# Kernel optimization log

Measured on AMD Instinct MI355X. Metric: run time of the kernel, lower is better.

Reference implementation:

```python
import jax, jax.numpy as jnp
import numpy as np

B, WIN, NN, F_IN, H = 8, 12, 2000, 8, 64
N = B * WIN * NN          # total graph nodes = 192000
E = 2_000_000             # edges
EPS = 1e-5                # BatchNorm eps
FC1_IN = 2 * H + WIN * F_IN + 1  # 225


def setup_inputs() -> dict:
    key = jax.random.key(0)
    ks = jax.random.split(key, 24)
    s = lambda k, shp: (jax.random.normal(k, shp, jnp.float32) * 0.05)
    d = {}
    d["adj_indices"] = jax.random.randint(ks[0], (2, E), 0, N)
    d["adj_weight"] = jax.random.uniform(ks[1], (E,), jnp.float32)
    d["x"] = jax.random.normal(ks[2], (N, F_IN), jnp.float32)
    d["inner_out"] = jax.random.normal(ks[3], (B * NN,), jnp.float32)
    # GCN layers
    d["W1"] = s(ks[4], (F_IN, H)); d["b1"] = jnp.zeros((H,), jnp.float32)
    d["W2"] = s(ks[5], (H, H));    d["b2"] = jnp.zeros((H,), jnp.float32)
    # BatchNorm affine params
    d["g1"] = jnp.ones((H,), jnp.float32);  d["be1"] = jnp.zeros((H,), jnp.float32)
    d["g2"] = jnp.ones((H,), jnp.float32);  d["be2"] = jnp.zeros((H,), jnp.float32)
    # LSTM 1 (input 2H) and LSTM 2 (input H); torch gate order i,f,g,o
    d["Wih1"] = s(ks[6], (4 * H, 2 * H)); d["Whh1"] = s(ks[7], (4 * H, H))
    d["bih1"] = jnp.zeros((4 * H,), jnp.float32); d["bhh1"] = jnp.zeros((4 * H,), jnp.float32)
    d["Wih2"] = s(ks[8], (4 * H, H)); d["Whh2"] = s(ks[9], (4 * H, H))
    d["bih2"] = jnp.zeros((4 * H,), jnp.float32); d["bhh2"] = jnp.zeros((4 * H,), jnp.float32)
    # FC head
    d["fc1_w"] = s(ks[10], (FC1_IN, H)); d["fc1_b"] = jnp.zeros((H,), jnp.float32)
    d["fc3_w"] = s(ks[11], (H, 1));      d["fc3_b"] = jnp.zeros((1,), jnp.float32)
    return d


def gcn(x, W, b, row, col, w):
    # PyG GCNConv: add self loops (weight 1), symmetric deg^-1/2 normalization,
    # aggregate messages from row (source) into col (target).
    loop = jnp.arange(N)
    r = jnp.concatenate([row, loop])
    c = jnp.concatenate([col, loop])
    ww = jnp.concatenate([w, jnp.ones((N,), w.dtype)])
    deg = jax.ops.segment_sum(ww, c, num_segments=N)
    dis = jnp.where(deg > 0, 1.0 / jnp.sqrt(deg), 0.0)
    norm = dis[r] * ww * dis[c]                      # [E+N]
    h = x @ W                                        # [N,H]
    out = jax.ops.segment_sum(h[r] * norm[:, None], c, num_segments=N)
    return out + b


def bn(x, g, b):  # training-mode BatchNorm1d (batch stats, biased var)
    m = x.mean(0)
    v = x.var(0)
    return (x - m) / jnp.sqrt(v + EPS) * g + b


def lstm(xs, Wih, Whh, bih, bhh):
    # xs: [T, Bn, D]; returns (all hidden states [T,Bn,H], last hidden [Bn,H])
    Bn = xs.shape[1]
    h0 = jnp.zeros((Bn, H), xs.dtype)
    def step(carry, xt):
        h, c = carry
        gates = xt @ Wih.T + h @ Whh.T + bih + bhh
        i, f, g, o = jnp.split(gates, 4, axis=-1)
        c = jax.nn.sigmoid(f) * c + jax.nn.sigmoid(i) * jnp.tanh(g)
        h = jax.nn.sigmoid(o) * jnp.tanh(c)
        return (h, c), h
    (hT, _), ys = jax.lax.scan(step, (h0, h0), xs)
    return ys, hT


def reference(adj_indices, adj_weight, x, inner_out,
              W1, b1, W2, b2, g1, be1, g2, be2,
              Wih1, Whh1, bih1, bhh1, Wih2, Whh2, bih2, bhh2,
              fc1_w, fc1_b, fc3_w, fc3_b):
    row, col = adj_indices[0], adj_indices[1]
    skip = x.reshape(B, WIN, NN, F_IN).transpose(0, 2, 1, 3).reshape(B * NN, WIN * F_IN)
    h1 = bn(jax.nn.relu(gcn(x, W1, b1, row, col, adj_weight)), g1, be1)   # dropout = identity (eval)
    h2 = bn(jax.nn.relu(gcn(h1, W2, b2, row, col, adj_weight)), g2, be2)
    h = jnp.concatenate([h1, h2], axis=1)                                  # [N, 2H]
    seq = h.reshape(B, WIN, NN, 2 * H).transpose(1, 0, 2, 3).reshape(WIN, B * NN, 2 * H)
    y1, hn1 = lstm(seq, Wih1, Whh1, bih1, bhh1)
    _, hn2 = lstm(y1, Wih2, Whh2, bih2, bhh2)
    z = jnp.concatenate([hn1, hn2, inner_out[:, None], skip], axis=1)      # [B*NN, FC1_IN]
    z = jax.nn.relu(z @ fc1_w + fc1_b)
    z = jax.nn.relu(z @ fc3_w + fc3_b)
    return z.reshape(-1)                                                   # [B*NN]
```

## Files before the change

kernel.cpp:

```cpp
#include <hip/hip_runtime.h>
#include <math.h>

#define N_NODES 192000
#define EDGES   2000000
#define HID     64
#define BN_ROWS 16000
#define T_WIN   12
#define B_SZ    8
#define NN_SZ   2000
#define FIN     8
#define BN_EPS  1e-5f

#define NBKT    750
#define NBLKA   1024
#define ACHUNK  1956
#define BKT_CAP 5120

typedef _Float16 f16x2 __attribute__((ext_vector_type(2)));
typedef _Float16 half4 __attribute__((ext_vector_type(4)));
typedef _Float16 half8 __attribute__((ext_vector_type(8)));
typedef float    f32x4 __attribute__((ext_vector_type(4)));
union F16x2U { float f; f16x2 h; };

__device__ __forceinline__ float frcp(float x){
#if __has_builtin(__builtin_amdgcn_rcpf)
    return __builtin_amdgcn_rcpf(x);
#else
    return 1.0f/x;
#endif
}
__device__ __forceinline__ float fsig(float x){ return frcp(1.0f + __expf(-x)); }
__device__ __forceinline__ float ftanh(float x){ return fmaf(2.0f, fsig(2.0f*x), -1.0f); }

__device__ __forceinline__ float packf16(float a, float b){
    F16x2U u; u.h[0] = (_Float16)a; u.h[1] = (_Float16)b; return u.f;
}

__global__ __launch_bounds__(256) void hist_coarse(
        const int* __restrict__ col, unsigned* __restrict__ gcount,
        int* __restrict__ blockbase){
    __shared__ unsigned bh[NBKT];
    int bl = blockIdx.x, tid = threadIdx.x;
    for (int i = tid; i < NBKT; i += 256) bh[i] = 0u;
    __syncthreads();
    int e0 = bl*ACHUNK;
    int e1 = e0 + ACHUNK; if (e1 > EDGES) e1 = EDGES;
    for (int e = e0 + tid*4; e < e1; e += 1024){
        int4 c4 = *(const int4*)&col[e];
        atomicAdd(&bh[((unsigned)c4.x) >> 8], 1u);
        atomicAdd(&bh[((unsigned)c4.y) >> 8], 1u);
        atomicAdd(&bh[((unsigned)c4.z) >> 8], 1u);
        atomicAdd(&bh[((unsigned)c4.w) >> 8], 1u);
    }
    __syncthreads();
    for (int i = tid; i < NBKT; i += 256)
        blockbase[bl*NBKT + i] = (int)atomicAdd(&gcount[i], bh[i]);
}

__global__ __launch_bounds__(1024) void scan_bkt(
        const unsigned* __restrict__ gcount, int* __restrict__ gbase,
        int* __restrict__ offsets){
    __shared__ int sm[1024];
    int tid = threadIdx.x;
    int v = (tid < NBKT) ? (int)gcount[tid] : 0;
    sm[tid] = v;
    __syncthreads();
    #pragma unroll
    for (int off = 1; off < 1024; off <<= 1){
        int t = (tid >= off) ? sm[tid - off] : 0;
        __syncthreads();
        sm[tid] += t;
        __syncthreads();
    }
    if (tid < NBKT) gbase[tid] = sm[tid] - v;
    if (tid == NBKT) gbase[NBKT] = EDGES;
    if (tid == NBKT+1) offsets[N_NODES] = EDGES;
}

__global__ __launch_bounds__(256) void scatter_bucket(
        const int* __restrict__ row, const int* __restrict__ col,
        const float* __restrict__ w, const int* __restrict__ blockbase,
        const int* __restrict__ gbase, int2* __restrict__ rec){
    __shared__ unsigned cur[NBKT];
    int bl = blockIdx.x, tid = threadIdx.x;
    for (int i = tid; i < NBKT; i += 256)
        cur[i] = (unsigned)(gbase[i] + blockbase[bl*NBKT + i]);
    __syncthreads();
    int e0 = bl*ACHUNK;
    int e1 = e0 + ACHUNK; if (e1 > EDGES) e1 = EDGES;
    for (int e = e0 + tid*4; e < e1; e += 1024){
        int4 r4 = *(const int4*)&row[e];
        int4 c4 = *(const int4*)&col[e];
        float4 w4 = *(const float4*)&w[e];
        int cc[4] = {c4.x, c4.y, c4.z, c4.w};
        int rr[4] = {r4.x, r4.y, r4.z, r4.w};
        float wf[4] = {w4.x, w4.y, w4.z, w4.w};
        #pragma unroll
        for (int q = 0; q < 4; q++){
            int c = cc[q];
            unsigned wfix = (unsigned)(wf[q]*16777216.0f + 0.5f);
            if (wfix > 0xFFFFFFu) wfix = 0xFFFFFFu;
            unsigned p = atomicAdd(&cur[((unsigned)c) >> 8], 1u);
            int2 rv; rv.x = rr[q];
            rv.y = (int)((((unsigned)(c & 255)) << 24) | wfix);
            rec[p] = rv;
        }
    }
}

__global__ __launch_bounds__(256) void bucket_csr(
        const int2* __restrict__ rec, const int* __restrict__ gbase,
        int2* __restrict__ edge_s, int* __restrict__ offsets,
        float* __restrict__ dis){
    __shared__ int2 S[BKT_CAP];
    __shared__ unsigned cnt[256];
    __shared__ unsigned wsum[256];
    __shared__ unsigned cur[256];
    __shared__ float dloc[256];
    int b = blockIdx.x, tid = threadIdx.x;
    int k0 = gbase[b], k1 = gbase[b+1];
    int n = k1 - k0;
    cnt[tid] = 0u; wsum[tid] = 0u;
    __syncthreads();
    bool staged = (n <= BKT_CAP);
    for (int i = tid; i < n; i += 256){
        int2 r = rec[k0 + i];
        if (staged) S[i] = r;
        unsigned clow = ((unsigned)r.y) >> 24;
        atomicAdd(&cnt[clow], 1u);
        atomicAdd(&wsum[clow], ((unsigned)r.y) & 0xFFFFFFu);
    }
    __syncthreads();
    unsigned v = cnt[tid];
    float deg = (float)wsum[tid] * (1.0f/16777216.0f);
    float dv = rsqrtf(deg + 1.0f);
    dloc[tid] = dv;
    dis[(b<<8) + tid] = dv;
    #pragma unroll
    for (int off = 1; off < 256; off <<= 1){
        unsigned t = (tid >= off) ? cnt[tid - off] : 0u;
        __syncthreads();
        cnt[tid] += t;
        __syncthreads();
    }
    unsigned excl = cnt[tid] - v;
    cur[tid] = excl;
    offsets[(b<<8) + tid] = k0 + (int)excl;
    __syncthreads();
    for (int i = tid; i < n; i += 256){
        int2 r = staged ? S[i] : rec[k0 + i];
        unsigned clow = ((unsigned)r.y) >> 24;
        unsigned wfix = ((unsigned)r.y) & 0xFFFFFFu;
        float sv = (float)wfix * (1.0f/16777216.0f) * dloc[clow];
        unsigned p = atomicAdd(&cur[clow], 1u);
        int2 o; o.x = (int)((clow << 24) | (unsigned)r.x); o.y = __float_as_int(sv);
        edge_s[k0 + (int)p] = o;
    }
}

__global__ __launch_bounds__(256) void edge_fix(
        int2* __restrict__ edge_s, const float* __restrict__ dis){
    int i = blockIdx.x*256 + threadIdx.x;
    if (i >= EDGES) return;
    int2 e = edge_s[i];
    e.y = __float_as_int(dis[e.x & 0xFFFFFF]*__int_as_float(e.y));
    edge_s[i] = e;
}

__global__ __launch_bounds__(256) void aggx_k(
        const int* __restrict__ offsets, const int2* __restrict__ edge_s,
        const float* __restrict__ dis, const float* __restrict__ x,
        float* __restrict__ ax){
    int g   = blockIdx.x*32 + (threadIdx.x >> 3);
    int sub = threadIdx.x & 7;
    float d = dis[g];
    float acc = x[(size_t)g*8 + sub]*d*d;
    int k  = offsets[g];
    int k1 = offsets[g+1];
    for (; k+4 <= k1; k += 4){
        int2 e0 = edge_s[k], e1 = edge_s[k+1], e2 = edge_s[k+2], e3 = edge_s[k+3];
        float v0 = x[(size_t)(e0.x & 0xFFFFFF)*8 + sub];
        float v1 = x[(size_t)(e1.x & 0xFFFFFF)*8 + sub];
        float v2 = x[(size_t)(e2.x & 0xFFFFFF)*8 + sub];
        float v3 = x[(size_t)(e3.x & 0xFFFFFF)*8 + sub];
        acc += v0*__int_as_float(e0.y);
        acc += v1*__int_as_float(e1.y);
        acc += v2*__int_as_float(e2.y);
        acc += v3*__int_as_float(e3.y);
    }
    for (; k < k1; k++){
        int2 e0 = edge_s[k];
        acc += x[(size_t)(e0.x & 0xFFFFFF)*8 + sub]*__int_as_float(e0.y);
    }
    ax[(size_t)g*8 + sub] = acc;
}

__global__ __launch_bounds__(256) void lin1b_stats(
        const float* __restrict__ ax, const float* __restrict__ W1,
        const float* __restrict__ b1, float* __restrict__ out,
        float* __restrict__ gsum, float* __restrict__ gsq){
    __shared__ float Ws[512];
    for (int i = threadIdx.x; i < 512; i += 256) Ws[i] = W1[i];
    __syncthreads();
    int f = threadIdx.x & 63;
    float wc[8];
    #pragma unroll
    for (int q = 0; q < 8; q++) wc[q] = Ws[q*64 + f];
    float bb = b1[f];
    float s = 0.f, s2 = 0.f;
    int stride = gridDim.x*blockDim.x;
    for (int idx = blockIdx.x*blockDim.x + threadIdx.x; idx < N_NODES*64; idx += stride){
        int j = idx >> 6;
        const float* ar = ax + (size_t)j*8;
        float acc = bb;
        #pragma unroll
        for (int q = 0; q < 8; q++) acc += ar[q]*wc[q];
        float v = fmaxf(acc, 0.f);
        out[idx] = v;
        s += v; s2 += v*v;
    }
    __shared__ float s1m[256], s2m[256];
    s1m[threadIdx.x] = s; s2m[threadIdx.x] = s2;
    __syncthreads();
    if (threadIdx.x < 64){
        float t1 = s1m[threadIdx.x]+s1m[threadIdx.x+64]+s1m[threadIdx.x+128]+s1m[threadIdx.x+192];
        float t2 = s2m[threadIdx.x]+s2m[threadIdx.x+64]+s2m[threadIdx.x+128]+s2m[threadIdx.x+192];
        atomicAdd(&gsum[threadIdx.x], t1);
        atomicAdd(&gsq[threadIdx.x], t2);
    }
}

#define L2ROWS 128
#define XS2    132
__global__ __launch_bounds__(128) void lin2_bn(
        const float* __restrict__ gcnA, const float* __restrict__ gsum,
        const float* __restrict__ gsq, const float* __restrict__ g1,
        const float* __restrict__ be1, const float* __restrict__ W2,
        _Float16* __restrict__ h1H, float* __restrict__ hlinH){
    __shared__ float Ws[64*64];
    __shared__ float xsT[64*XS2];
    int tid = threadIdx.x;
    int r0 = blockIdx.x * L2ROWS;

    for (int i = tid; i < 1024; i += 128)
        *(float4*)&Ws[i*4] = *(const float4*)&W2[i*4];

    int k4 = tid & 15;
    int rb = tid >> 4;
    float scv[4], shv[4];
    #pragma unroll
    for (int q = 0; q < 4; q++){
        int f = k4*4 + q;
        float mean = gsum[f]*(1.0f/(float)N_NODES);
        float var  = fmaxf(gsq[f]*(1.0f/(float)N_NODES) - mean*mean, 0.f);
        float sc_  = g1[f]*rsqrtf(var + BN_EPS);
        scv[q] = sc_; shv[q] = be1[f] - mean*sc_;
    }
    for (int it = 0; it < 16; it++){
        int r = it*8 + rb;
        float4 v = *(const float4*)&gcnA[(size_t)(r0+r)*64 + k4*4];
        v.x = v.x*scv[0]+shv[0]; v.y = v.y*scv[1]+shv[1];
        v.z = v.z*scv[2]+shv[2]; v.w = v.w*scv[3]+shv[3];
        half4 hh;
        hh[0]=(_Float16)v.x; hh[1]=(_Float16)v.y; hh[2]=(_Float16)v.z; hh[3]=(_Float16)v.w;
        *(half4*)&h1H[(size_t)(r0+r)*64 + k4*4] = hh;
        xsT[(k4*4+0)*XS2 + r] = v.x;
        xsT[(k4*4+1)*XS2 + r] = v.y;
        xsT[(k4*4+2)*XS2 + r] = v.z;
        xsT[(k4*4+3)*XS2 + r] = v.w;
    }
    __syncthreads();

    int cg = tid & 7;
    int rg = tid >> 3;
    float acc[8][8];
    #pragma unroll
    for (int i = 0; i < 8; i++)
        #pragma unroll
        for (int j = 0; j < 8; j++) acc[i][j] = 0.f;

    float4 a0 = *(float4*)&xsT[0*XS2 + rg*8];
    float4 a1 = *(float4*)&xsT[0*XS2 + rg*8 + 4];
    float4 w0 = *(float4*)&Ws[0*64 + cg*8];
    float4 w1 = *(float4*)&Ws[0*64 + cg*8 + 4];
    for (int k = 0; k < 64; k++){
        float4 na0, na1, nw0, nw1;
        if (k < 63){
            na0 = *(float4*)&xsT[(k+1)*XS2 + rg*8];
            na1 = *(float4*)&xsT[(k+1)*XS2 + rg*8 + 4];
            nw0 = *(float4*)&Ws[(k+1)*64 + cg*8];
            nw1 = *(float4*)&Ws[(k+1)*64 + cg*8 + 4];
        }
        float ar[8] = {a0.x,a0.y,a0.z,a0.w,a1.x,a1.y,a1.z,a1.w};
        float wcv[8] = {w0.x,w0.y,w0.z,w0.w,w1.x,w1.y,w1.z,w1.w};
        #pragma unroll
        for (int i = 0; i < 8; i++)
            #pragma unroll
            for (int j = 0; j < 8; j++) acc[i][j] += ar[i]*wcv[j];
        a0=na0; a1=na1; w0=nw0; w1=nw1;
    }
    #pragma unroll
    for (int i = 0; i < 8; i++){
        size_t r = (size_t)(r0 + rg*8 + i);
        float4 pk;
        pk.x = packf16(acc[i][0], acc[i][1]);
        pk.y = packf16(acc[i][2], acc[i][3]);
        pk.z = packf16(acc[i][4], acc[i][5]);
        pk.w = packf16(acc[i][6], acc[i][7]);
        *(float4*)&hlinH[r*32 + cg*4] = pk;
    }
}

__global__ __launch_bounds__(256) void gather2h(
        const int* __restrict__ offsets, const int2* __restrict__ edge_s,
        const float* __restrict__ dis, const float* __restrict__ hlinH,
        const float* __restrict__ bias, float* __restrict__ g2Hf){
    int j = blockIdx.x*8 + (threadIdx.x >> 5);
    int p = threadIdx.x & 31;
    float d = dis[j];
    float dd = d*d;
    F16x2U u; u.f = hlinH[(size_t)j*32 + p];
    float ax = (float)u.h[0]*dd;
    float ay = (float)u.h[1]*dd;
    int k  = offsets[j];
    int k1 = offsets[j+1];
    for (; k+4 <= k1; k += 4){
        int2 e0 = edge_s[k], e1 = edge_s[k+1], e2 = edge_s[k+2], e3 = edge_s[k+3];
        F16x2U a, b, c, e;
        a.f = hlinH[(size_t)(e0.x & 0xFFFFFF)*32 + p];
        b.f = hlinH[(size_t)(e1.x & 0xFFFFFF)*32 + p];
        c.f = hlinH[(size_t)(e2.x & 0xFFFFFF)*32 + p];
        e.f = hlinH[(size_t)(e3.x & 0xFFFFFF)*32 + p];
        float n0 = __int_as_float(e0.y), n1 = __int_as_float(e1.y);
        float n2 = __int_as_float(e2.y), n3 = __int_as_float(e3.y);
        ax += (float)a.h[0]*n0; ay += (float)a.h[1]*n0;
        ax += (float)b.h[0]*n1; ay += (float)b.h[1]*n1;
        ax += (float)c.h[0]*n2; ay += (float)c.h[1]*n2;
        ax += (float)e.h[0]*n3; ay += (float)e.h[1]*n3;
    }
    for (; k < k1; k++){
        int2 e0 = edge_s[k];
        F16x2U a; a.f = hlinH[(size_t)(e0.x & 0xFFFFFF)*32 + p];
        float n0 = __int_as_float(e0.y);
        ax += (float)a.h[0]*n0; ay += (float)a.h[1]*n0;
    }
    float2 bv = *(const float2*)&bias[2*p];
    float vx = fmaxf(ax + bv.x, 0.f);
    float vy = fmaxf(ay + bv.y, 0.f);
    F16x2U o; o.h[0] = (_Float16)vx; o.h[1] = (_Float16)vy;
    g2Hf[(size_t)j*32 + p] = o.f;
}

__global__ __launch_bounds__(256) void stats2h(
        const float* __restrict__ g2Hf, float* __restrict__ gsum2, float* __restrict__ gsq2){
    int p = threadIdx.x & 31;
    float s0 = 0.f, s1 = 0.f, q0 = 0.f, q1 = 0.f;
    int stride = gridDim.x*blockDim.x;
    for (int idx = blockIdx.x*blockDim.x + threadIdx.x; idx < N_NODES*32; idx += stride){
        F16x2U u; u.f = g2Hf[idx];
        float vx = (float)u.h[0], vy = (float)u.h[1];
        s0 += vx; q0 += vx*vx;
        s1 += vy; q1 += vy*vy;
    }
    __shared__ float sb[128];
    if (threadIdx.x < 128) sb[threadIdx.x] = 0.f;
    __syncthreads();
    atomicAdd(&sb[2*p],      s0);
    atomicAdd(&sb[2*p+1],    s1);
    atomicAdd(&sb[64+2*p],   q0);
    atomicAdd(&sb[64+2*p+1], q1);
    __syncthreads();
    if (threadIdx.x < 64){
        atomicAdd(&gsum2[threadIdx.x], sb[threadIdx.x]);
        atomicAdd(&gsq2[threadIdx.x],  sb[64+threadIdx.x]);
    }
}

__global__ void prep_weights(const float* __restrict__ Wih1, const float* __restrict__ Whh1,
                             const float* __restrict__ bih1, const float* __restrict__ bhh1,
                             const float* __restrict__ Wih2, const float* __restrict__ Whh2,
                             const float* __restrict__ bih2, const float* __restrict__ bhh2,
                             _Float16* W1F, _Float16* W2F, float* b1c, float* b2c){
    int idx = blockIdx.x*blockDim.x + threadIdx.x;
    if (idx < 6*256*32){
        int kt = idx >> 13;
        int rem = idx & 8191;
        int n = rem >> 5, kin = rem & 31;
        int k = kt*32 + kin;
        float v = (k < 128) ? Wih1[n*128 + k] : Whh1[n*64 + (k-128)];
        W1F[idx] = (_Float16)v;
    }
    int i2 = idx - 6*256*32;
    if (i2 >= 0 && i2 < 4*256*32){
        int kt = i2 >> 13;
        int rem = i2 & 8191;
        int n = rem >> 5, kin = rem & 31;
        int k = kt*32 + kin;
        float v = (k < 64) ? Wih2[n*64 + k] : Whh2[n*64 + (k-64)];
        W2F[i2] = (_Float16)v;
    }
    int i3 = idx - (6*256*32 + 4*256*32);
    if (i3 >= 0 && i3 < 256) b1c[i3] = bih1[i3] + bhh1[i3];
    int i4 = i3 - 256;
    if (i4 >= 0 && i4 < 256) b2c[i4] = bih2[i4] + bhh2[i4];
}

#define X1S 200
#define X2S 136
__global__ __launch_bounds__(256) void lstm_fused(
        const _Float16* __restrict__ h1H, const _Float16* __restrict__ g2H,
        const float* __restrict__ gsum2, const float* __restrict__ gsq2,
        const float* __restrict__ g2bn, const float* __restrict__ be2,
        const _Float16* __restrict__ W1F, const _Float16* __restrict__ W2F,
        const float* __restrict__ b1c, const float* __restrict__ b2c,
        float* __restrict__ h1s, float* __restrict__ h2s){
    __shared__ _Float16 X1h[16*X1S];
    __shared__ _Float16 X2h[16*X2S];
    int tid = threadIdx.x;
    int j0 = blockIdx.x*16;
    int w    = tid >> 6;
    int lane = tid & 63;
    int quad = lane >> 4;
    int l16  = lane & 15;
    int u    = 16*w + l16;

    int c4 = tid & 15;
    int sr = (tid >> 4) & 15;
    int sj = j0 + sr;
    int sb = sj / NN_SZ, sn = sj - sb*NN_SZ;
    size_t rbase = ((size_t)(sb*T_WIN)*NN_SZ + sn)*64 + c4*4;
    float sc2v[4], sh2v[4];
    #pragma unroll
    for (int q = 0; q < 4; q++){
        int f = c4*4 + q;
        float mean = gsum2[f]*(1.0f/(float)N_NODES);
        float var  = fmaxf(gsq2[f]*(1.0f/(float)N_NODES) - mean*mean, 0.f);
        float sc_  = g2bn[f]*rsqrtf(var + BN_EPS);
        sc2v[q] = sc_; sh2v[q] = be2[f] - mean*sc_;
    }

    float c1r[4], c2r[4], h2r[4];
    #pragma unroll
    for (int i = 0; i < 4; i++){ c1r[i] = 0.f; c2r[i] = 0.f; h2r[i] = 0.f; }

    float bi1 = b1c[u], bf1 = b1c[64+u], bg1 = b1c[128+u], bo1 = b1c[192+u];
    float bi2 = b2c[u], bf2 = b2c[64+u], bg2 = b2c[128+u], bo2 = b2c[192+u];

    {
        half4 v0 = *(const half4*)&h1H[rbase];
        half4 g4 = *(const half4*)&g2H[rbase];
        half4 v1;
        #pragma unroll
        for (int q = 0; q < 4; q++) v1[q] = (_Float16)((float)g4[q]*sc2v[q] + sh2v[q]);
        *(half4*)&X1h[sr*X1S + c4*4]       = v0;
        *(half4*)&X1h[sr*X1S + 64 + c4*4]  = v1;
        *(half4*)&X1h[sr*X1S + 128 + c4*4] = (half4){0,0,0,0};
    }
    __syncthreads();

    for (int t = 0; t < T_WIN; t++){
        half4 nv0, ng4;
        if (t < T_WIN-1){
            size_t rb = rbase + (size_t)(t+1)*NN_SZ*64;
            nv0 = *(const half4*)&h1H[rb];
            ng4 = *(const half4*)&g2H[rb];
        }

        f32x4 acc[4];
        #pragma unroll
        for (int g = 0; g < 4; g++) acc[g] = (f32x4){0.f,0.f,0.f,0.f};
        #pragma unroll
        for (int kt = 0; kt < 6; kt++){
            half8 a = *(const half8*)&X1h[l16*X1S + kt*32 + quad*8];
            #pragma unroll
            for (int g = 0; g < 4; g++){
                half8 b = *(const half8*)&W1F[(size_t)(kt*256 + 64*g + u)*32 + quad*8];
                acc[g] = __builtin_amdgcn_mfma_f32_16x16x32_f16(a, b, acc[g], 0, 0, 0);
            }
        }
        __syncthreads();

        #pragma unroll
        for (int r = 0; r < 4; r++){
            int rowl = quad*4 + r;
            float gi = acc[0][r] + bi1;
            float gf = acc[1][r] + bf1;
            float gg = acc[2][r] + bg1;
            float go = acc[3][r] + bo1;
            float cn = fsig(gf)*c1r[r] + fsig(gi)*ftanh(gg);
            float hn = fsig(go)*ftanh(cn);
            c1r[r] = cn;
            X2h[rowl*X2S + u]      = (_Float16)hn;
            X2h[rowl*X2S + 64 + u] = (_Float16)h2r[r];
            X1h[rowl*X1S + 128 + u] = (_Float16)hn;
            if (t == T_WIN-1) h1s[(size_t)(j0 + rowl)*64 + u] = hn;
        }
        if (t < T_WIN-1){
            half4 v1;
            #pragma unroll
            for (int q = 0; q < 4; q++) v1[q] = (_Float16)((float)ng4[q]*sc2v[q] + sh2v[q]);
            *(half4*)&X1h[sr*X1S + c4*4]      = nv0;
            *(half4*)&X1h[sr*X1S + 64 + c4*4] = v1;
        }
        __syncthreads();

        f32x4 acc2[4];
        #pragma unroll
        for (int g = 0; g < 4; g++) acc2[g] = (f32x4){0.f,0.f,0.f,0.f};
        #pragma unroll
        for (int kt = 0; kt < 4; kt++){
            half8 a = *(const half8*)&X2h[l16*X2S + kt*32 + quad*8];
            #pragma unroll
            for (int g = 0; g < 4; g++){
                half8 b = *(const half8*)&W2F[(size_t)(kt*256 + 64*g + u)*32 + quad*8];
                acc2[g] = __builtin_amdgcn_mfma_f32_16x16x32_f16(a, b, acc2[g], 0, 0, 0);
            }
        }

        #pragma unroll
        for (int r = 0; r < 4; r++){
            int rowl = quad*4 + r;
            float gi = acc2[0][r] + bi2;
            float gf = acc2[1][r] + bf2;
            float gg = acc2[2][r] + bg2;
            float go = acc2[3][r] + bo2;
            float cn = fsig(gf)*c2r[r] + fsig(gi)*ftanh(gg);
            float hn = fsig(go)*ftanh(cn);
            c2r[r] = cn;
            h2r[r] = hn;
            if (t == T_WIN-1) h2s[(size_t)(j0 + rowl)*64 + u] = hn;
        }
    }
}

__global__ __launch_bounds__(256) void fc_head(
        const float* __restrict__ h1s, const float* __restrict__ h2s,
        const float* __restrict__ inner, const float* __restrict__ x,
        const float* __restrict__ fc1_w, const float* __restrict__ fc1_b,
        const float* __restrict__ fc3_w, const float* __restrict__ fc3_b,
        float* __restrict__ out){
    __shared__ float zsm[4][226];
    int wv = threadIdx.x >> 6;
    int f  = threadIdx.x & 63;
    int j  = blockIdx.x*4 + wv;
    int b = j / NN_SZ, n = j - b*NN_SZ;
    for (int k = f; k < 225; k += 64){
        float v;
        if (k < 64)        v = h1s[j*64 + k];
        else if (k < 128)  v = h2s[j*64 + (k-64)];
        else if (k == 128) v = inner[j];
        else {
            int kk = k - 129;
            int w_ = kk >> 3, ff = kk & 7;
            v = x[((b*T_WIN + w_)*NN_SZ + n)*FIN + ff];
        }
        zsm[wv][k] = v;
    }
    __syncthreads();
    float acc = fc1_b[f];
    for (int k = 0; k < 225; k++) acc += zsm[wv][k]*fc1_w[k*64 + f];
    float p = fmaxf(acc, 0.f) * fc3_w[f];
    #pragma unroll
    for (int off = 32; off > 0; off >>= 1) p += __shfl_down(p, off, 64);
    if (f == 0) out[j] = fmaxf(p + fc3_b[0], 0.f);
}

extern "C" void kernel_launch(void* const* d_in, const int* in_sizes, int n_in,
                              void* d_out, int out_size, void* d_ws, size_t ws_size,
                              hipStream_t stream){
    const int*   adj  = (const int*)d_in[0];
    const int*   row  = adj;
    const int*   col  = adj + EDGES;
    const float* aw   = (const float*)d_in[1];
    const float* x    = (const float*)d_in[2];
    const float* inner= (const float*)d_in[3];
    const float* W1   = (const float*)d_in[4];
    const float* b1   = (const float*)d_in[5];
    const float* W2   = (const float*)d_in[6];
    const float* b2   = (const float*)d_in[7];
    const float* g1   = (const float*)d_in[8];
    const float* be1  = (const float*)d_in[9];
    const float* g2   = (const float*)d_in[10];
    const float* be2  = (const float*)d_in[11];
    const float* Wih1 = (const float*)d_in[12];
    const float* Whh1 = (const float*)d_in[13];
    const float* bih1 = (const float*)d_in[14];
    const float* bhh1 = (const float*)d_in[15];
    const float* Wih2 = (const float*)d_in[16];
    const float* Whh2 = (const float*)d_in[17];
    const float* bih2 = (const float*)d_in[18];
    const float* bhh2 = (const float*)d_in[19];
    const float* fc1w = (const float*)d_in[20];
    const float* fc1b = (const float*)d_in[21];
    const float* fc3w = (const float*)d_in[22];
    const float* fc3b = (const float*)d_in[23];
    float* out = (float*)d_out;

    float* ws = (float*)d_ws;
    const size_t NB = (size_t)N_NODES*64;
    float* bufX = ws;
    float* bufY = ws + NB;
    float* bufZ = ws + 2*NB;
    int2*  edge_s  = (int2*)(ws + 3*NB);
    float* degdis  = ws + 3*NB + (size_t)2*EDGES;
    float* gsum    = degdis + N_NODES;
    float* gsq     = gsum + 64;
    float* gsum2   = gsq + 64;
    float* gsq2    = gsum2 + 64;
    unsigned* gcount = (unsigned*)(gsq2 + 64);
    int* gbase   = (int*)(gcount + NBKT);
    int* offsets = gbase + (NBKT + 2);

    int* blockbase = (int*)bufX;
    int2* rec      = (int2*)bufY;

    float* hlinH = bufX;
    _Float16* h1H = (_Float16*)bufZ;
    float* ax    = bufZ + (size_t)N_NODES*32 + 64;
    float* gcnA1 = bufY;
    float* g2Hf  = bufY;

    float* h1s = bufX;
    float* h2s = bufX + (size_t)BN_ROWS*64;
    _Float16* W1F = (_Float16*)(bufX + (size_t)4*BN_ROWS*64);
    _Float16* W2F = W1F + 6*256*32;
    float* b1c = (float*)(W2F + 4*256*32);
    float* b2c = b1c + 256;

    hipMemsetAsync(gcount, 0, NBKT*sizeof(unsigned), stream);
    hipMemsetAsync(gsum, 0, 256*sizeof(float), stream);
    hist_coarse   <<<NBLKA, 256, 0, stream>>>(col, gcount, blockbase);
    scan_bkt      <<<1, 1024, 0, stream>>>(gcount, gbase, offsets);
    scatter_bucket<<<NBLKA, 256, 0, stream>>>(row, col, aw, blockbase, gbase, rec);
    bucket_csr    <<<NBKT, 256, 0, stream>>>(rec, gbase, edge_s, offsets, degdis);
    edge_fix      <<<(EDGES+255)/256, 256, 0, stream>>>(edge_s, degdis);

    aggx_k<<<N_NODES/32, 256, 0, stream>>>(offsets, edge_s, degdis, x, ax);
    lin1b_stats<<<1024, 256, 0, stream>>>(ax, W1, b1, gcnA1, gsum, gsq);

    lin2_bn<<<N_NODES/L2ROWS, 128, 0, stream>>>(gcnA1, gsum, gsq, g1, be1, W2, h1H, hlinH);

    gather2h<<<N_NODES/8, 256, 0, stream>>>(offsets, edge_s, degdis, hlinH, b2, g2Hf);
    stats2h<<<1024, 256, 0, stream>>>(g2Hf, gsum2, gsq2);

    prep_weights<<<(6*256*32 + 4*256*32 + 512 + 255)/256, 256, 0, stream>>>(
        Wih1, Whh1, bih1, bhh1, Wih2, Whh2, bih2, bhh2, W1F, W2F, b1c, b2c);
    lstm_fused<<<BN_ROWS/16, 256, 0, stream>>>(h1H, (const _Float16*)g2Hf,
                                               gsum2, gsq2, g2, be2,
                                               W1F, W2F, b1c, b2c, h1s, h2s);

    fc_head<<<BN_ROWS/4, 256, 0, stream>>>(h1s, h2s, inner, x, fc1w, fc1b, fc3w, fc3b, out);
}
```

Measured before the change: 519.4 us.

## Split degree pass, fold edge_fix into CSR build, double LSTM rows per block

Degree computation moves into its own bucket_deg kernel. bucket_csr can then apply both source and target normalisation when it writes each edge, which removes the separate edge_fix pass over all edges. The LSTM kernel now handles 32 nodes per block instead of 16, so each weight fragment loaded for the MFMAs is reused across two row tiles. The scatter/histogram grid also shrinks from 1024 to 256 blocks with larger chunks, which gives fewer blocks on the GPU and more register and LDS pressure per LSTM block.

```diff
diff --git a/kernel.cpp b/kernel.cpp
--- a/kernel.cpp
+++ b/kernel.cpp
@@ -12,8 +12,8 @@
 #define BN_EPS  1e-5f
 
 #define NBKT    750
-#define NBLKA   1024
-#define ACHUNK  1956
+#define NBLKA   256
+#define ACHUNK  7824
 #define BKT_CAP 5120
 
 typedef _Float16 f16x2 __attribute__((ext_vector_type(2)));
@@ -108,34 +108,45 @@
     }
 }
 
+__global__ __launch_bounds__(256) void bucket_deg(
+        const int2* __restrict__ rec, const int* __restrict__ gbase,
+        float* __restrict__ dis){
+    __shared__ unsigned wsum[256];
+    int b = blockIdx.x, tid = threadIdx.x;
+    wsum[tid] = 0u;
+    __syncthreads();
+    int k0 = gbase[b], k1 = gbase[b+1];
+    for (int i = k0 + tid; i < k1; i += 256){
+        int2 r = rec[i];
+        atomicAdd(&wsum[((unsigned)r.y) >> 24], ((unsigned)r.y) & 0xFFFFFFu);
+    }
+    __syncthreads();
+    float deg = (float)wsum[tid] * (1.0f/16777216.0f);
+    dis[(b<<8) + tid] = rsqrtf(deg + 1.0f);
+}
+
 __global__ __launch_bounds__(256) void bucket_csr(
         const int2* __restrict__ rec, const int* __restrict__ gbase,
-        int2* __restrict__ edge_s, int* __restrict__ offsets,
-        float* __restrict__ dis){
+        const float* __restrict__ dis,
+        int2* __restrict__ edge_s, int* __restrict__ offsets){
     __shared__ int2 S[BKT_CAP];
     __shared__ unsigned cnt[256];
-    __shared__ unsigned wsum[256];
     __shared__ unsigned cur[256];
     __shared__ float dloc[256];
     int b = blockIdx.x, tid = threadIdx.x;
     int k0 = gbase[b], k1 = gbase[b+1];
     int n = k1 - k0;
-    cnt[tid] = 0u; wsum[tid] = 0u;
+    cnt[tid] = 0u;
+    dloc[tid] = dis[(b<<8) + tid];
     __syncthreads();
     bool staged = (n <= BKT_CAP);
     for (int i = tid; i < n; i += 256){
         int2 r = rec[k0 + i];
         if (staged) S[i] = r;
-        unsigned clow = ((unsigned)r.y) >> 24;
-        atomicAdd(&cnt[clow], 1u);
-        atomicAdd(&wsum[clow], ((unsigned)r.y) & 0xFFFFFFu);
+        atomicAdd(&cnt[((unsigned)r.y) >> 24], 1u);
     }
     __syncthreads();
     unsigned v = cnt[tid];
-    float deg = (float)wsum[tid] * (1.0f/16777216.0f);
-    float dv = rsqrtf(deg + 1.0f);
-    dloc[tid] = dv;
-    dis[(b<<8) + tid] = dv;
     #pragma unroll
     for (int off = 1; off < 256; off <<= 1){
         unsigned t = (tid >= off) ? cnt[tid - off] : 0u;
@@ -152,19 +163,11 @@
         unsigned clow = ((unsigned)r.y) >> 24;
         unsigned wfix = ((unsigned)r.y) & 0xFFFFFFu;
         float sv = (float)wfix * (1.0f/16777216.0f) * dloc[clow];
+        sv = dis[r.x] * sv;
         unsigned p = atomicAdd(&cur[clow], 1u);
         int2 o; o.x = (int)((clow << 24) | (unsigned)r.x); o.y = __float_as_int(sv);
         edge_s[k0 + (int)p] = o;
     }
-}
-
-__global__ __launch_bounds__(256) void edge_fix(
-        int2* __restrict__ edge_s, const float* __restrict__ dis){
-    int i = blockIdx.x*256 + threadIdx.x;
-    if (i >= EDGES) return;
-    int2 e = edge_s[i];
-    e.y = __float_as_int(dis[e.x & 0xFFFFFF]*__int_as_float(e.y));
-    edge_s[i] = e;
 }
 
 __global__ __launch_bounds__(256) void aggx_k(
@@ -414,10 +417,10 @@
         const _Float16* __restrict__ W1F, const _Float16* __restrict__ W2F,
         const float* __restrict__ b1c, const float* __restrict__ b2c,
         float* __restrict__ h1s, float* __restrict__ h2s){
-    __shared__ _Float16 X1h[16*X1S];
-    __shared__ _Float16 X2h[16*X2S];
+    __shared__ _Float16 X1h[32*X1S];
+    __shared__ _Float16 X2h[32*X2S];
     int tid = threadIdx.x;
-    int j0 = blockIdx.x*16;
+    int j0 = blockIdx.x*32;
     int w    = tid >> 6;
     int lane = tid & 63;
     int quad = lane >> 4;
@@ -426,9 +429,13 @@
 
     int c4 = tid & 15;
     int sr = (tid >> 4) & 15;
-    int sj = j0 + sr;
-    int sb = sj / NN_SZ, sn = sj - sb*NN_SZ;
-    size_t rbase = ((size_t)(sb*T_WIN)*NN_SZ + sn)*64 + c4*4;
+    int sjA = j0 + sr;
+    int sjB = sjA + 16;
+    int sbA = sjA / NN_SZ, snA = sjA - sbA*NN_SZ;
+    int sbB = sjB / NN_SZ, snB = sjB - sbB*NN_SZ;
+    size_t rbaseA = ((size_t)(sbA*T_WIN)*NN_SZ + snA)*64 + c4*4;
+    size_t rbaseB = ((size_t)(sbB*T_WIN)*NN_SZ + snB)*64 + c4*4;
+    const size_t tstep = (size_t)NN_SZ*64;
     float sc2v[4], sh2v[4];
     #pragma unroll
     for (int q = 0; q < 4; q++){
@@ -439,96 +446,128 @@
         sc2v[q] = sc_; sh2v[q] = be2[f] - mean*sc_;
     }
 
-    float c1r[4], c2r[4], h2r[4];
-    #pragma unroll
-    for (int i = 0; i < 4; i++){ c1r[i] = 0.f; c2r[i] = 0.f; h2r[i] = 0.f; }
+    float c1r[2][4], c2r[2][4], h2r[2][4];
+    #pragma unroll
+    for (int tle = 0; tle < 2; tle++)
+        #pragma unroll
+        for (int i = 0; i < 4; i++){ c1r[tle][i] = 0.f; c2r[tle][i] = 0.f; h2r[tle][i] = 0.f; }
 
     float bi1 = b1c[u], bf1 = b1c[64+u], bg1 = b1c[128+u], bo1 = b1c[192+u];
     float bi2 = b2c[u], bf2 = b2c[64+u], bg2 = b2c[128+u], bo2 = b2c[192+u];
 
     {
-        half4 v0 = *(const half4*)&h1H[rbase];
-        half4 g4 = *(const half4*)&g2H[rbase];
-        half4 v1;
-        #pragma unroll
-        for (int q = 0; q < 4; q++) v1[q] = (_Float16)((float)g4[q]*sc2v[q] + sh2v[q]);
-        *(half4*)&X1h[sr*X1S + c4*4]       = v0;
-        *(half4*)&X1h[sr*X1S + 64 + c4*4]  = v1;
-        *(half4*)&X1h[sr*X1S + 128 + c4*4] = (half4){0,0,0,0};
+        half4 v0A = *(const half4*)&h1H[rbaseA];
+        half4 g4A = *(const half4*)&g2H[rbaseA];
+        half4 v0B = *(const half4*)&h1H[rbaseB];
+        half4 g4B = *(const half4*)&g2H[rbaseB];
+        half4 v1A, v1B;
+        #pragma unroll
+        for (int q = 0; q < 4; q++){
+            v1A[q] = (_Float16)((float)g4A[q]*sc2v[q] + sh2v[q]);
+            v1B[q] = (_Float16)((float)g4B[q]*sc2v[q] + sh2v[q]);
+        }
+        *(half4*)&X1h[sr*X1S + c4*4]             = v0A;
+        *(half4*)&X1h[sr*X1S + 64 + c4*4]        = v1A;
+        *(half4*)&X1h[sr*X1S + 128 + c4*4]       = (half4){0,0,0,0};
+        *(half4*)&X1h[(sr+16)*X1S + c4*4]        = v0B;
+        *(half4*)&X1h[(sr+16)*X1S + 64 + c4*4]   = v1B;
+        *(half4*)&X1h[(sr+16)*X1S + 128 + c4*4]  = (half4){0,0,0,0};
     }
     __syncthreads();
 
     for (int t = 0; t < T_WIN; t++){
-        half4 nv0, ng4;
+        half4 nv0A, ng4A, nv0B, ng4B;
         if (t < T_WIN-1){
-            size_t rb = rbase + (size_t)(t+1)*NN_SZ*64;
-            nv0 = *(const half4*)&h1H[rb];
-            ng4 = *(const half4*)&g2H[rb];
-        }
-
-        f32x4 acc[4];
-        #pragma unroll
-        for (int g = 0; g < 4; g++) acc[g] = (f32x4){0.f,0.f,0.f,0.f};
+            size_t rbA = rbaseA + (size_t)(t+1)*tstep;
+            size_t rbB = rbaseB + (size_t)(t+1)*tstep;
+            nv0A = *(const half4*)&h1H[rbA];
+            ng4A = *(const half4*)&g2H[rbA];
+            nv0B = *(const half4*)&h1H[rbB];
+            ng4B = *(const half4*)&g2H[rbB];
+        }
+
+        f32x4 acc[2][4];
+        #pragma unroll
+        for (int tle = 0; tle < 2; tle++)
+            #pragma unroll
+            for (int g = 0; g < 4; g++) acc[tle][g] = (f32x4){0.f,0.f,0.f,0.f};
         #pragma unroll
         for (int kt = 0; kt < 6; kt++){
-            half8 a = *(const half8*)&X1h[l16*X1S + kt*32 + quad*8];
+            half8 a0 = *(const half8*)&X1h[l16*X1S + kt*32 + quad*8];
+            half8 a1 = *(const half8*)&X1h[(l16+16)*X1S + kt*32 + quad*8];
             #pragma unroll
             for (int g = 0; g < 4; g++){
                 half8 b = *(const half8*)&W1F[(size_t)(kt*256 + 64*g + u)*32 + quad*8];
-                acc[g] = __builtin_amdgcn_mfma_f32_16x16x32_f16(a, b, acc[g], 0, 0, 0);
+                acc[0][g] = __builtin_amdgcn_mfma_f32_16x16x32_f16(a0, b, acc[0][g], 0, 0, 0);
+                acc[1][g] = __builtin_amdgcn_mfma_f32_16x16x32_f16(a1, b, acc[1][g], 0, 0, 0);
             }
         }
         __syncthreads();
 
         #pragma unroll
-        for (int r = 0; r < 4; r++){
-            int rowl = quad*4 + r;
-            float gi = acc[0][r] + bi1;
-            float gf = acc[1][r] + bf1;
-            float gg = acc[2][r] + bg1;
-            float go = acc[3][r] + bo1;
-            float cn = fsig(gf)*c1r[r] + fsig(gi)*ftanh(gg);
-            float hn = fsig(go)*ftanh(cn);
-            c1r[r] = cn;
-            X2h[rowl*X2S + u]      = (_Float16)hn;
-            X2h[rowl*X2S + 64 + u] = (_Float16)h2r[r];
-            X1h[rowl*X1S + 128 + u] = (_Float16)hn;
-            if (t == T_WIN-1) h1s[(size_t)(j0 + rowl)*64 + u] = hn;
+        for (int tle = 0; tle < 2; tle++){
+            #pragma unroll
+            for (int r = 0; r < 4; r++){
+                int rowl = quad*4 + r + 16*tle;
+                float gi = acc[tle][0][r] + bi1;
+                float gf = acc[tle][1][r] + bf1;
+                float gg = acc[tle][2][r] + bg1;
+                float go = acc[tle][3][r] + bo1;
+                float cn = fsig(gf)*c1r[tle][r] + fsig(gi)*ftanh(gg);
+                float hn = fsig(go)*ftanh(cn);
+                c1r[tle][r] = cn;
+                X2h[rowl*X2S + u]      = (_Float16)hn;
+                X2h[rowl*X2S + 64 + u] = (_Float16)h2r[tle][r];
+                X1h[rowl*X1S + 128 + u] = (_Float16)hn;
+                if (t == T_WIN-1) h1s[(size_t)(j0 + rowl)*64 + u] = hn;
+            }
         }
         if (t < T_WIN-1){
-            half4 v1;
-            #pragma unroll
-            for (int q = 0; q < 4; q++) v1[q] = (_Float16)((float)ng4[q]*sc2v[q] + sh2v[q]);
-            *(half4*)&X1h[sr*X1S + c4*4]      = nv0;
-            *(half4*)&X1h[sr*X1S + 64 + c4*4] = v1;
+            half4 v1A, v1B;
+            #pragma unroll
+            for (int q = 0; q < 4; q++){
+                v1A[q] = (_Float16)((float)ng4A[q]*sc2v[q] + sh2v[q]);
+                v1B[q] = (_Float16)((float)ng4B[q]*sc2v[q] + sh2v[q]);
+            }
+            *(half4*)&X1h[sr*X1S + c4*4]            = nv0A;
+            *(half4*)&X1h[sr*X1S + 64 + c4*4]       = v1A;
+            *(half4*)&X1h[(sr+16)*X1S + c4*4]       = nv0B;
+            *(half4*)&X1h[(sr+16)*X1S + 64 + c4*4]  = v1B;
         }
         __syncthreads();
 
-        f32x4 acc2[4];
-        #pragma unroll
-        for (int g = 0; g < 4; g++) acc2[g] = (f32x4){0.f,0.f,0.f,0.f};
+        f32x4 acc2[2][4];
+        #pragma unroll
+        for (int tle = 0; tle < 2; tle++)
+            #pragma unroll
+            for (int g = 0; g < 4; g++) acc2[tle][g] = (f32x4){0.f,0.f,0.f,0.f};
         #pragma unroll
         for (int kt = 0; kt < 4; kt++){
-            half8 a = *(const half8*)&X2h[l16*X2S + kt*32 + quad*8];
+            half8 a0 = *(const half8*)&X2h[l16*X2S + kt*32 + quad*8];
+            half8 a1 = *(const half8*)&X2h[(l16+16)*X2S + kt*32 + quad*8];
             #pragma unroll
             for (int g = 0; g < 4; g++){
                 half8 b = *(const half8*)&W2F[(size_t)(kt*256 + 64*g + u)*32 + quad*8];
-                acc2[g] = __builtin_amdgcn_mfma_f32_16x16x32_f16(a, b, acc2[g], 0, 0, 0);
+                acc2[0][g] = __builtin_amdgcn_mfma_f32_16x16x32_f16(a0, b, acc2[0][g], 0, 0, 0);
+                acc2[1][g] = __builtin_amdgcn_mfma_f32_16x16x32_f16(a1, b, acc2[1][g], 0, 0, 0);
             }
         }
 
         #pragma unroll
-        for (int r = 0; r < 4; r++){
-            int rowl = quad*4 + r;
-            float gi = acc2[0][r] + bi2;
-            float gf = acc2[1][r] + bf2;
-            float gg = acc2[2][r] + bg2;
-            float go = acc2[3][r] + bo2;
-            float cn = fsig(gf)*c2r[r] + fsig(gi)*ftanh(gg);
-            float hn = fsig(go)*ftanh(cn);
-            c2r[r] = cn;
-            h2r[r] = hn;
-            if (t == T_WIN-1) h2s[(size_t)(j0 + rowl)*64 + u] = hn;
+        for (int tle = 0; tle < 2; tle++){
+            #pragma unroll
+            for (int r = 0; r < 4; r++){
+                int rowl = quad*4 + r + 16*tle;
+                float gi = acc2[tle][0][r] + bi2;
+                float gf = acc2[tle][1][r] + bf2;
+                float gg = acc2[tle][2][r] + bg2;
+                float go = acc2[tle][3][r] + bo2;
+                float cn = fsig(gf)*c2r[tle][r] + fsig(gi)*ftanh(gg);
+                float hn = fsig(go)*ftanh(cn);
+                c2r[tle][r] = cn;
+                h2r[tle][r] = hn;
+                if (t == T_WIN-1) h2s[(size_t)(j0 + rowl)*64 + u] = hn;
+            }
         }
     }
 }
@@ -632,8 +671,8 @@
     hist_coarse   <<<NBLKA, 256, 0, stream>>>(col, gcount, blockbase);
     scan_bkt      <<<1, 1024, 0, stream>>>(gcount, gbase, offsets);
     scatter_bucket<<<NBLKA, 256, 0, stream>>>(row, col, aw, blockbase, gbase, rec);
-    bucket_csr    <<<NBKT, 256, 0, stream>>>(rec, gbase, edge_s, offsets, degdis);
-    edge_fix      <<<(EDGES+255)/256, 256, 0, stream>>>(edge_s, degdis);
+    bucket_deg    <<<NBKT, 256, 0, stream>>>(rec, gbase, degdis);
+    bucket_csr    <<<NBKT, 256, 0, stream>>>(rec, gbase, degdis, edge_s, offsets);
 
     aggx_k<<<N_NODES/32, 256, 0, stream>>>(offsets, edge_s, degdis, x, ax);
     lin1b_stats<<<1024, 256, 0, stream>>>(ax, W1, b1, gcnA1, gsum, gsq);
@@ -645,7 +684,7 @@
 
     prep_weights<<<(6*256*32 + 4*256*32 + 512 + 255)/256, 256, 0, stream>>>(
         Wih1, Whh1, bih1, bhh1, Wih2, Whh2, bih2, bhh2, W1F, W2F, b1c, b2c);
-    lstm_fused<<<BN_ROWS/16, 256, 0, stream>>>(h1H, (const _Float16*)g2Hf,
+    lstm_fused<<<BN_ROWS/32, 256, 0, stream>>>(h1H, (const _Float16*)g2Hf,
                                                gsum2, gsq2, g2, be2,
                                                W1F, W2F, b1c, b2c, h1s, h2s);
 
```

Result: faster. 489.4 us (-5.8%).

## Split degree pass, fold edge_fix into CSR build, register-resident LSTM weights

Applied to the files above, without the earlier changes.

Computes node degrees in a separate bucket_deg pass so bucket_csr can apply both source and target normalization directly, which removes the edge_fix kernel's extra read-write pass over the edge array. It also launches fewer, larger blocks for the histogram and scatter kernels. The LSTM kernel now handles 32 rows per 512-thread block, with each wave keeping half of the gate weights in registers and swapping partial gate results through shared memory. This cuts repeated global weight loads but adds a barrier per step, more register pressure and more LDS use.

```diff
diff --git a/kernel.cpp b/kernel.cpp
--- a/kernel.cpp
+++ b/kernel.cpp
@@ -12,8 +12,8 @@
 #define BN_EPS  1e-5f
 
 #define NBKT    750
-#define NBLKA   1024
-#define ACHUNK  1956
+#define NBLKA   256
+#define ACHUNK  7824
 #define BKT_CAP 5120
 
 typedef _Float16 f16x2 __attribute__((ext_vector_type(2)));
@@ -108,34 +108,45 @@
     }
 }
 
+__global__ __launch_bounds__(256) void bucket_deg(
+        const int2* __restrict__ rec, const int* __restrict__ gbase,
+        float* __restrict__ dis){
+    __shared__ unsigned wsum[256];
+    int b = blockIdx.x, tid = threadIdx.x;
+    wsum[tid] = 0u;
+    __syncthreads();
+    int k0 = gbase[b], k1 = gbase[b+1];
+    for (int i = k0 + tid; i < k1; i += 256){
+        int2 r = rec[i];
+        atomicAdd(&wsum[((unsigned)r.y) >> 24], ((unsigned)r.y) & 0xFFFFFFu);
+    }
+    __syncthreads();
+    float deg = (float)wsum[tid] * (1.0f/16777216.0f);
+    dis[(b<<8) + tid] = rsqrtf(deg + 1.0f);
+}
+
 __global__ __launch_bounds__(256) void bucket_csr(
         const int2* __restrict__ rec, const int* __restrict__ gbase,
-        int2* __restrict__ edge_s, int* __restrict__ offsets,
-        float* __restrict__ dis){
+        const float* __restrict__ dis,
+        int2* __restrict__ edge_s, int* __restrict__ offsets){
     __shared__ int2 S[BKT_CAP];
     __shared__ unsigned cnt[256];
-    __shared__ unsigned wsum[256];
     __shared__ unsigned cur[256];
     __shared__ float dloc[256];
     int b = blockIdx.x, tid = threadIdx.x;
     int k0 = gbase[b], k1 = gbase[b+1];
     int n = k1 - k0;
-    cnt[tid] = 0u; wsum[tid] = 0u;
+    cnt[tid] = 0u;
+    dloc[tid] = dis[(b<<8) + tid];
     __syncthreads();
     bool staged = (n <= BKT_CAP);
     for (int i = tid; i < n; i += 256){
         int2 r = rec[k0 + i];
         if (staged) S[i] = r;
-        unsigned clow = ((unsigned)r.y) >> 24;
-        atomicAdd(&cnt[clow], 1u);
-        atomicAdd(&wsum[clow], ((unsigned)r.y) & 0xFFFFFFu);
+        atomicAdd(&cnt[((unsigned)r.y) >> 24], 1u);
     }
     __syncthreads();
     unsigned v = cnt[tid];
-    float deg = (float)wsum[tid] * (1.0f/16777216.0f);
-    float dv = rsqrtf(deg + 1.0f);
-    dloc[tid] = dv;
-    dis[(b<<8) + tid] = dv;
     #pragma unroll
     for (int off = 1; off < 256; off <<= 1){
         unsigned t = (tid >= off) ? cnt[tid - off] : 0u;
@@ -152,19 +163,11 @@
         unsigned clow = ((unsigned)r.y) >> 24;
         unsigned wfix = ((unsigned)r.y) & 0xFFFFFFu;
         float sv = (float)wfix * (1.0f/16777216.0f) * dloc[clow];
+        sv = dis[r.x] * sv;
         unsigned p = atomicAdd(&cur[clow], 1u);
         int2 o; o.x = (int)((clow << 24) | (unsigned)r.x); o.y = __float_as_int(sv);
         edge_s[k0 + (int)p] = o;
     }
-}
-
-__global__ __launch_bounds__(256) void edge_fix(
-        int2* __restrict__ edge_s, const float* __restrict__ dis){
-    int i = blockIdx.x*256 + threadIdx.x;
-    if (i >= EDGES) return;
-    int2 e = edge_s[i];
-    e.y = __float_as_int(dis[e.x & 0xFFFFFF]*__int_as_float(e.y));
-    edge_s[i] = e;
 }
 
 __global__ __launch_bounds__(256) void aggx_k(
@@ -407,28 +410,35 @@
 
 #define X1S 200
 #define X2S 136
-__global__ __launch_bounds__(256) void lstm_fused(
+#define EXS 130
+__global__ __launch_bounds__(512) void lstm_fused(
         const _Float16* __restrict__ h1H, const _Float16* __restrict__ g2H,
         const float* __restrict__ gsum2, const float* __restrict__ gsq2,
         const float* __restrict__ g2bn, const float* __restrict__ be2,
         const _Float16* __restrict__ W1F, const _Float16* __restrict__ W2F,
         const float* __restrict__ b1c, const float* __restrict__ b2c,
         float* __restrict__ h1s, float* __restrict__ h2s){
-    __shared__ _Float16 X1h[16*X1S];
-    __shared__ _Float16 X2h[16*X2S];
+    __shared__ _Float16 X1h[32*X1S];
+    __shared__ _Float16 X2h[32*X2S];
+    __shared__ float EX1[32*EXS];
+    __shared__ float EX2[32*EXS];
     int tid = threadIdx.x;
-    int j0 = blockIdx.x*16;
+    int j0 = blockIdx.x*32;
     int w    = tid >> 6;
     int lane = tid & 63;
     int quad = lane >> 4;
     int l16  = lane & 15;
-    int u    = 16*w + l16;
-
+    int ug   = w & 3;
+    int gp   = w >> 2;
+    int u    = ug*16 + l16;
+    int row0 = gp*16 + quad*4;
+
+    int sr = tid >> 4;
     int c4 = tid & 15;
-    int sr = (tid >> 4) & 15;
     int sj = j0 + sr;
     int sb = sj / NN_SZ, sn = sj - sb*NN_SZ;
     size_t rbase = ((size_t)(sb*T_WIN)*NN_SZ + sn)*64 + c4*4;
+    const size_t tstep = (size_t)NN_SZ*64;
     float sc2v[4], sh2v[4];
     #pragma unroll
     for (int q = 0; q < 4; q++){
@@ -439,12 +449,24 @@
         sc2v[q] = sc_; sh2v[q] = be2[f] - mean*sc_;
     }
 
-    float c1r[4], c2r[4], h2r[4];
-    #pragma unroll
-    for (int i = 0; i < 4; i++){ c1r[i] = 0.f; c2r[i] = 0.f; h2r[i] = 0.f; }
-
     float bi1 = b1c[u], bf1 = b1c[64+u], bg1 = b1c[128+u], bo1 = b1c[192+u];
     float bi2 = b2c[u], bf2 = b2c[64+u], bg2 = b2c[128+u], bo2 = b2c[192+u];
+
+    half8 w1r[6][2], w2r[4][2];
+    #pragma unroll
+    for (int kt = 0; kt < 6; kt++)
+        #pragma unroll
+        for (int gg = 0; gg < 2; gg++)
+            w1r[kt][gg] = *(const half8*)&W1F[(size_t)(kt*256 + 64*(2*gp+gg) + u)*32 + quad*8];
+    #pragma unroll
+    for (int kt = 0; kt < 4; kt++)
+        #pragma unroll
+        for (int gg = 0; gg < 2; gg++)
+            w2r[kt][gg] = *(const half8*)&W2F[(size_t)(kt*256 + 64*(2*gp+gg) + u)*32 + quad*8];
+
+    float c1r[4], c2r[4], h2r[4];
+    #pragma unroll
+    for (int i = 0; i < 4; i++){ c1r[i] = 0.f; c2r[i] = 0.f; h2r[i] = 0.f; }
 
     {
         half4 v0 = *(const half4*)&h1H[rbase];
@@ -461,33 +483,46 @@
     for (int t = 0; t < T_WIN; t++){
         half4 nv0, ng4;
         if (t < T_WIN-1){
-            size_t rb = rbase + (size_t)(t+1)*NN_SZ*64;
+            size_t rb = rbase + (size_t)(t+1)*tstep;
             nv0 = *(const half4*)&h1H[rb];
             ng4 = *(const half4*)&g2H[rb];
         }
 
-        f32x4 acc[4];
-        #pragma unroll
-        for (int g = 0; g < 4; g++) acc[g] = (f32x4){0.f,0.f,0.f,0.f};
+        f32x4 a1acc0[2], a1acc1[2];
+        #pragma unroll
+        for (int gg = 0; gg < 2; gg++){ a1acc0[gg] = (f32x4){0,0,0,0}; a1acc1[gg] = (f32x4){0,0,0,0}; }
         #pragma unroll
         for (int kt = 0; kt < 6; kt++){
-            half8 a = *(const half8*)&X1h[l16*X1S + kt*32 + quad*8];
+            half8 a0 = *(const half8*)&X1h[l16*X1S + kt*32 + quad*8];
+            half8 a1 = *(const half8*)&X1h[(l16+16)*X1S + kt*32 + quad*8];
             #pragma unroll
-            for (int g = 0; g < 4; g++){
-                half8 b = *(const half8*)&W1F[(size_t)(kt*256 + 64*g + u)*32 + quad*8];
-                acc[g] = __builtin_amdgcn_mfma_f32_16x16x32_f16(a, b, acc[g], 0, 0, 0);
+            for (int gg = 0; gg < 2; gg++){
+                a1acc0[gg] = __builtin_amdgcn_mfma_f32_16x16x32_f16(a0, w1r[kt][gg], a1acc0[gg], 0, 0, 0);
+                a1acc1[gg] = __builtin_amdgcn_mfma_f32_16x16x32_f16(a1, w1r[kt][gg], a1acc1[gg], 0, 0, 0);
             }
         }
+        #pragma unroll
+        for (int gg = 0; gg < 2; gg++)
+            #pragma unroll
+            for (int r = 0; r < 4; r++){
+                float v = gp ? a1acc0[gg][r] : a1acc1[gg][r];
+                int xrow = (gp^1)*16 + quad*4 + r;
+                EX1[xrow*EXS + gg*64 + u] = v;
+            }
         __syncthreads();
 
         #pragma unroll
         for (int r = 0; r < 4; r++){
-            int rowl = quad*4 + r;
-            float gi = acc[0][r] + bi1;
-            float gf = acc[1][r] + bf1;
-            float gg = acc[2][r] + bg1;
-            float go = acc[3][r] + bo1;
-            float cn = fsig(gf)*c1r[r] + fsig(gi)*ftanh(gg);
+            int rowl = row0 + r;
+            float own0 = gp ? a1acc1[0][r] : a1acc0[0][r];
+            float own1 = gp ? a1acc1[1][r] : a1acc0[1][r];
+            float oth0 = EX1[rowl*EXS + 0*64 + u];
+            float oth1 = EX1[rowl*EXS + 1*64 + u];
+            float gi = (gp ? oth0 : own0) + bi1;
+            float gf = (gp ? oth1 : own1) + bf1;
+            float gG = (gp ? own0 : oth0) + bg1;
+            float go = (gp ? own1 : oth1) + bo1;
+            float cn = fsig(gf)*c1r[r] + fsig(gi)*ftanh(gG);
             float hn = fsig(go)*ftanh(cn);
             c1r[r] = cn;
             X2h[rowl*X2S + u]      = (_Float16)hn;
@@ -504,27 +539,41 @@
         }
         __syncthreads();
 
-        f32x4 acc2[4];
-        #pragma unroll
-        for (int g = 0; g < 4; g++) acc2[g] = (f32x4){0.f,0.f,0.f,0.f};
+        f32x4 a2acc0[2], a2acc1[2];
+        #pragma unroll
+        for (int gg = 0; gg < 2; gg++){ a2acc0[gg] = (f32x4){0,0,0,0}; a2acc1[gg] = (f32x4){0,0,0,0}; }
         #pragma unroll
         for (int kt = 0; kt < 4; kt++){
-            half8 a = *(const half8*)&X2h[l16*X2S + kt*32 + quad*8];
+            half8 a0 = *(const half8*)&X2h[l16*X2S + kt*32 + quad*8];
+            half8 a1 = *(const half8*)&X2h[(l16+16)*X2S + kt*32 + quad*8];
             #pragma unroll
-            for (int g = 0; g < 4; g++){
-                half8 b = *(const half8*)&W2F[(size_t)(kt*256 + 64*g + u)*32 + quad*8];
-                acc2[g] = __builtin_amdgcn_mfma_f32_16x16x32_f16(a, b, acc2[g], 0, 0, 0);
+            for (int gg = 0; gg < 2; gg++){
+                a2acc0[gg] = __builtin_amdgcn_mfma_f32_16x16x32_f16(a0, w2r[kt][gg], a2acc0[gg], 0, 0, 0);
+                a2acc1[gg] = __builtin_amdgcn_mfma_f32_16x16x32_f16(a1, w2r[kt][gg], a2acc1[gg], 0, 0, 0);
             }
         }
+        #pragma unroll
+        for (int gg = 0; gg < 2; gg++)
+            #pragma unroll
+            for (int r = 0; r < 4; r++){
+                float v = gp ? a2acc0[gg][r] : a2acc1[gg][r];
+                int xrow = (gp^1)*16 + quad*4 + r;
+                EX2[xrow*EXS + gg*64 + u] = v;
+            }
+        __syncthreads();
 
         #pragma unroll
         for (int r = 0; r < 4; r++){
-            int rowl = quad*4 + r;
-            float gi = acc2[0][r] + bi2;
-            float gf = acc2[1][r] + bf2;
-            float gg = acc2[2][r] + bg2;
-            float go = acc2[3][r] + bo2;
-            float cn = fsig(gf)*c2r[r] + fsig(gi)*ftanh(gg);
+            int rowl = row0 + r;
+            float own0 = gp ? a2acc1[0][r] : a2acc0[0][r];
+            float own1 = gp ? a2acc1[1][r] : a2acc0[1][r];
+            float oth0 = EX2[rowl*EXS + 0*64 + u];
+            float oth1 = EX2[rowl*EXS + 1*64 + u];
+            float gi = (gp ? oth0 : own0) + bi2;
+            float gf = (gp ? oth1 : own1) + bf2;
+            float gG = (gp ? own0 : oth0) + bg2;
+            float go = (gp ? own1 : oth1) + bo2;
+            float cn = fsig(gf)*c2r[r] + fsig(gi)*ftanh(gG);
             float hn = fsig(go)*ftanh(cn);
             c2r[r] = cn;
             h2r[r] = hn;
@@ -632,8 +681,8 @@
     hist_coarse   <<<NBLKA, 256, 0, stream>>>(col, gcount, blockbase);
     scan_bkt      <<<1, 1024, 0, stream>>>(gcount, gbase, offsets);
     scatter_bucket<<<NBLKA, 256, 0, stream>>>(row, col, aw, blockbase, gbase, rec);
-    bucket_csr    <<<NBKT, 256, 0, stream>>>(rec, gbase, edge_s, offsets, degdis);
-    edge_fix      <<<(EDGES+255)/256, 256, 0, stream>>>(edge_s, degdis);
+    bucket_deg    <<<NBKT, 256, 0, stream>>>(rec, gbase, degdis);
+    bucket_csr    <<<NBKT, 256, 0, stream>>>(rec, gbase, degdis, edge_s, offsets);
 
     aggx_k<<<N_NODES/32, 256, 0, stream>>>(offsets, edge_s, degdis, x, ax);
     lin1b_stats<<<1024, 256, 0, stream>>>(ax, W1, b1, gcnA1, gsum, gsq);
@@ -645,7 +694,7 @@
 
     prep_weights<<<(6*256*32 + 4*256*32 + 512 + 255)/256, 256, 0, stream>>>(
         Wih1, Whh1, bih1, bhh1, Wih2, Whh2, bih2, bhh2, W1F, W2F, b1c, b2c);
-    lstm_fused<<<BN_ROWS/16, 256, 0, stream>>>(h1H, (const _Float16*)g2Hf,
+    lstm_fused<<<BN_ROWS/32, 512, 0, stream>>>(h1H, (const _Float16*)g2Hf,
                                                gsum2, gsq2, g2, be2,
                                                W1F, W2F, b1c, b2c, h1s, h2s);
 
```

Result: faster. 490.7 us (-5.5%).
